# Performance work log

Hardware: AMD Instinct MI355X
Metric: run time of the kernel (lower is better)

## Reference

```python
import jax, jax.numpy as jnp
import numpy as np

B, D_IN, D_STATE, N_SEG = 8192, 2048, 2048, 4


def setup_inputs() -> dict:
    key = jax.random.key(0)
    ks = jax.random.split(key, 7)
    s_in = 1.0 / np.sqrt(D_IN)
    return {
        "x": jax.random.normal(ks[0], (B, D_IN), dtype=jnp.float32),
        "W_seg": jax.random.uniform(ks[1], (N_SEG, D_STATE, D_IN), minval=-s_in, maxval=s_in, dtype=jnp.float32),
        "b_seg": jax.random.uniform(ks[2], (N_SEG, D_STATE), minval=-s_in, maxval=s_in, dtype=jnp.float32),
        "threshold": jnp.zeros((N_SEG, D_STATE), dtype=jnp.float32),
        "W_gate": jax.random.uniform(ks[3], (N_SEG, D_IN), minval=-s_in, maxval=s_in, dtype=jnp.float32),
        "b_gate": jax.random.uniform(ks[4], (N_SEG,), minval=-s_in, maxval=s_in, dtype=jnp.float32),
    }


def reference(x, W_seg, b_seg, threshold, W_gate, b_gate):
    # gates: (B, n_seg)
    gates = jax.nn.sigmoid(x @ W_gate.T + b_gate)
    # all segment projections in one batched GEMM: (n_seg, B, d_state)
    seg = jnp.einsum("bi,sdi->sbd", x, W_seg) + b_seg[:, None, :]
    plateau = jax.nn.sigmoid(5.0 * (seg - threshold[:, None, :]))
    # stacked: (n_seg, B, d_state), gated per segment
    stacked = seg * plateau * gates.T[:, :, None]
    n = stacked.shape[0]
    integrated = (
        stacked.sum(0)
        + 0.1 * jnp.sign(jnp.prod(stacked, 0)) * jnp.power(jnp.prod(jnp.abs(stacked), 0), 1.0 / n)
    )
    return integrated
```

## Files before the change

kernel.cpp:

```cpp
#include <hip/hip_runtime.h>
#include <stdint.h>

#define B_DIM 8192
#define K_DIM 2048
#define N_DIM 2048
#define NSEG 4
#define NT (K_DIM / 64)

typedef int v4i __attribute__((ext_vector_type(4)));

typedef const __attribute__((address_space(1))) void* gas_ptr;
typedef __attribute__((address_space(3))) void* lds_ptr;

__global__ __launch_bounds__(256)
void xquant_gates_kernel(const float* __restrict__ x, const float* __restrict__ Wg,
                         const float* __restrict__ bg, signed char* __restrict__ xq,
                         float* __restrict__ sx, float* __restrict__ gates) {
  const int b = blockIdx.x;
  const int tid = threadIdx.x;
  const size_t base = (size_t)b * K_DIM + tid * 8;
  const float4 v0 = *(const float4*)(x + base);
  const float4 v1 = *(const float4*)(x + base + 4);

  float a[4];
#pragma unroll
  for (int s = 0; s < 4; ++s) {
    const float4 w0 = *(const float4*)(Wg + (size_t)s * K_DIM + tid * 8);
    const float4 w1 = *(const float4*)(Wg + (size_t)s * K_DIM + tid * 8 + 4);
    a[s] = v0.x * w0.x + v0.y * w0.y + v0.z * w0.z + v0.w * w0.w
         + v1.x * w1.x + v1.y * w1.y + v1.z * w1.z + v1.w * w1.w;
  }
  float m = fmaxf(fmaxf(fmaxf(fabsf(v0.x), fabsf(v0.y)), fmaxf(fabsf(v0.z), fabsf(v0.w))),
                  fmaxf(fmaxf(fabsf(v1.x), fabsf(v1.y)), fmaxf(fabsf(v1.z), fabsf(v1.w))));
#pragma unroll
  for (int off = 1; off < 64; off <<= 1) {
    m = fmaxf(m, __shfl_xor(m, off));
#pragma unroll
    for (int s = 0; s < 4; ++s) a[s] += __shfl_xor(a[s], off);
  }
  __shared__ float redg[4][4];
  __shared__ float rmx[4];
  const int wv = tid >> 6;
  if ((tid & 63) == 0) {
    rmx[wv] = m;
#pragma unroll
    for (int s = 0; s < 4; ++s) redg[wv][s] = a[s];
  }
  __syncthreads();
  const float rm = fmaxf(fmaxf(rmx[0], rmx[1]), fmaxf(rmx[2], rmx[3]));
  const float inv = 127.0f / fmaxf(rm, 1e-30f);
  const int q0 = __float2int_rn(v0.x * inv), q1 = __float2int_rn(v0.y * inv);
  const int q2 = __float2int_rn(v0.z * inv), q3 = __float2int_rn(v0.w * inv);
  const int q4 = __float2int_rn(v1.x * inv), q5 = __float2int_rn(v1.y * inv);
  const int q6 = __float2int_rn(v1.z * inv), q7 = __float2int_rn(v1.w * inv);
  const int lo = (q0 & 255) | ((q1 & 255) << 8) | ((q2 & 255) << 16) | ((q3 & 255) << 24);
  const int hi = (q4 & 255) | ((q5 & 255) << 8) | ((q6 & 255) << 16) | ((q7 & 255) << 24);
  ((int2*)xq)[(size_t)b * 256 + tid] = make_int2(lo, hi);
  if (tid == 0) sx[b] = rm * (1.0f / 127.0f);
  if (tid < 4) {
    float v = redg[0][tid] + redg[1][tid] + redg[2][tid] + redg[3][tid] + bg[tid];
    gates[(size_t)b * 4 + tid] = 1.f / (1.f + __expf(-v));
  }
}

__global__ __launch_bounds__(256)
void wquant_kernel(const float* __restrict__ W, signed char* __restrict__ wq,
                   float* __restrict__ sw) {
  const int row = blockIdx.x;
  const int tid = threadIdx.x;
  const size_t base = (size_t)row * K_DIM + tid * 8;
  const float4 v0 = *(const float4*)(W + base);
  const float4 v1 = *(const float4*)(W + base + 4);
  float m = fmaxf(fmaxf(fmaxf(fabsf(v0.x), fabsf(v0.y)), fmaxf(fabsf(v0.z), fabsf(v0.w))),
                  fmaxf(fmaxf(fabsf(v1.x), fabsf(v1.y)), fmaxf(fabsf(v1.z), fabsf(v1.w))));
#pragma unroll
  for (int off = 1; off < 64; off <<= 1) m = fmaxf(m, __shfl_xor(m, off));
  __shared__ float rmx[4];
  if ((tid & 63) == 0) rmx[tid >> 6] = m;
  __syncthreads();
  const float rm = fmaxf(fmaxf(rmx[0], rmx[1]), fmaxf(rmx[2], rmx[3]));
  const float inv = 127.0f / fmaxf(rm, 1e-30f);
  const int q0 = __float2int_rn(v0.x * inv), q1 = __float2int_rn(v0.y * inv);
  const int q2 = __float2int_rn(v0.z * inv), q3 = __float2int_rn(v0.w * inv);
  const int q4 = __float2int_rn(v1.x * inv), q5 = __float2int_rn(v1.y * inv);
  const int q6 = __float2int_rn(v1.z * inv), q7 = __float2int_rn(v1.w * inv);
  const int lo = (q0 & 255) | ((q1 & 255) << 8) | ((q2 & 255) << 16) | ((q3 & 255) << 24);
  const int hi = (q4 & 255) | ((q5 & 255) << 8) | ((q6 & 255) << 16) | ((q7 & 255) << 24);
  ((int2*)wq)[(size_t)row * 256 + tid] = make_int2(lo, hi);
  if (tid == 0) sw[row] = rm * (1.0f / 127.0f);
}

__global__ __launch_bounds__(512, 4)
void seg_gemm_kernel(const signed char* __restrict__ Xq,
                     const signed char* __restrict__ Wq,
                     const float* __restrict__ sx,
                     const float* __restrict__ sw,
                     const float* __restrict__ b_seg,
                     const float* __restrict__ thr,
                     const float* __restrict__ gates,
                     float* __restrict__ out) {
  __shared__ __align__(128) char smem[65536];

  const int tid = threadIdx.x;
  const int lane = tid & 63;
  const int wid = tid >> 6;
  const int wm = wid >> 2;
  const int wn = wid & 3;

  const int id = blockIdx.x;
  const int x = id & 7;
  const int c = id >> 3;
  const int mIdx = (c >> 3) & 7;
  const int nIdx = (c & 7) | ((c >> 6) << 3);
  const int m0 = (x * 8 + mIdx) * 128;
  const int n0 = nIdx * 64;

  const int row_st = tid >> 2;
  const int kc    = (tid & 3) ^ ((tid >> 3) & 3);
  const int keOff = kc * 16;
  const int ldsd  = tid * 16;

  const int l15 = lane & 15;
  const int kg  = lane >> 4;
  const int aSw = l15 * 64 + ((kg ^ ((l15 >> 1) & 3)) << 4);

  v4i acc[NSEG][4];
#pragma unroll
  for (int s = 0; s < NSEG; ++s)
#pragma unroll
    for (int f = 0; f < 4; ++f) acc[s][f] = (v4i){0, 0, 0, 0};

#define STAGE_A(t_) do {                                                            \
    const signed char* s0_ = Xq + (size_t)(m0 + row_st) * K_DIM + (t_) * 64 + keOff; \
    __builtin_amdgcn_global_load_lds((gas_ptr)s0_, (lds_ptr)(smem + ((t_) & 1) * 8192 + ldsd), 16, 0, 0); \
  } while (0)

#define STAGE_B(t_, h_, bb_) do {                                                   \
    const signed char* s0_ = Wq + ((size_t)((h_) * 2 + (tid >> 8)) * N_DIM + (n0 + ((tid >> 2) & 63))) * K_DIM + (t_) * 64 + keOff; \
    __builtin_amdgcn_global_load_lds((gas_ptr)s0_, (lds_ptr)(smem + 16384 + (bb_) * 16384 + (h_) * 8192 + ldsd), 16, 0, 0); \
  } while (0)

#define MFMAI(a_, b_, c_) __builtin_amdgcn_mfma_i32_16x16x64_i8(a_, b_, c_, 0, 0, 0)
#define LD16(p_) (*(const v4i*)(p_))
#define WAITL(n_) asm volatile("s_waitcnt lgkmcnt(" #n_ ")" ::: "memory")

#define MM4(f_) do {                                                                \
    __builtin_amdgcn_s_setprio(1);                                                  \
    acc[0][(f_)] = MFMAI(a[(f_)], bfr[0], acc[0][(f_)]);                            \
    acc[1][(f_)] = MFMAI(a[(f_)], bfr[1], acc[1][(f_)]);                            \
    acc[2][(f_)] = MFMAI(a[(f_)], bfr[2], acc[2][(f_)]);                            \
    acc[3][(f_)] = MFMAI(a[(f_)], bfr[3], acc[3][(f_)]);                            \
    __builtin_amdgcn_s_setprio(0);                                                  \
  } while (0)

  STAGE_A(0);
  STAGE_B(0, 0, 0); STAGE_B(0, 1, 0);
  STAGE_B(1, 0, 1); STAGE_B(1, 1, 1);
  asm volatile("s_waitcnt vmcnt(2)" ::: "memory");
  __builtin_amdgcn_s_barrier();

  int bc = 0, bs = 2;
  for (int t = 0; t < NT; ++t) {
    const char* Ab = smem + (t & 1) * 8192 + wm * 4096;
    const char* Bb = smem + 16384 + bc * 16384;
    v4i bfr[NSEG];
    v4i a[4];

    bfr[0] = LD16(Bb + 0 * 4096 + wn * 1024 + aSw);
    bfr[1] = LD16(Bb + 1 * 4096 + wn * 1024 + aSw);
    bfr[2] = LD16(Bb + 2 * 4096 + wn * 1024 + aSw);
    bfr[3] = LD16(Bb + 3 * 4096 + wn * 1024 + aSw);
    a[0] = LD16(Ab + 0 * 1024 + aSw);
    a[1] = LD16(Ab + 1 * 1024 + aSw);
    a[2] = LD16(Ab + 2 * 1024 + aSw);
    a[3] = LD16(Ab + 3 * 1024 + aSw);
    if (t + 1 < NT) STAGE_A(t + 1);

    WAITL(3);  MM4(0);
    WAITL(2);
    if (t + 2 < NT) STAGE_B(t + 2, 0, bs);
    MM4(1);
    WAITL(1);
    if (t + 2 < NT) STAGE_B(t + 2, 1, bs);
    MM4(2);
    WAITL(0);  MM4(3);

    if (t < NT - 2)      { asm volatile("s_waitcnt vmcnt(2)" ::: "memory"); }
    else if (t == NT - 2){ asm volatile("s_waitcnt vmcnt(0)" ::: "memory"); }
    __builtin_amdgcn_s_barrier();

    bc = (bc == 2) ? 0 : bc + 1;
    bs = (bs == 2) ? 0 : bs + 1;
  }
  asm volatile("s_waitcnt lgkmcnt(0) vmcnt(0)" ::: "memory");

  const int d = n0 + wn * 16 + l15;
  float bsv[NSEG], thv[NSEG], swv[NSEG];
#pragma unroll
  for (int s = 0; s < NSEG; ++s) {
    bsv[s] = b_seg[s * N_DIM + d];
    thv[s] = thr[s * N_DIM + d];
    swv[s] = sw[s * N_DIM + d];
  }
#pragma unroll
  for (int f = 0; f < 4; ++f) {
#pragma unroll
    for (int r = 0; r < 4; ++r) {
      const int brow = m0 + wm * 64 + f * 16 + kg * 4 + r;
      const float sxr = sx[brow];
      const float4 g = *(const float4*)(gates + (size_t)brow * 4);
      const float gv[NSEG] = {g.x, g.y, g.z, g.w};
      float sum = 0.f, prod = 1.f;
#pragma unroll
      for (int s = 0; s < NSEG; ++s) {
        const float seg = (float)acc[s][f][r] * (sxr * swv[s]) + bsv[s];
        const float pl = 1.f / (1.f + __expf(-5.f * (seg - thv[s])));
        const float st = seg * pl * gv[s];
        sum += st;
        prod *= st;
      }
      const float gm = sqrtf(sqrtf(fabsf(prod)));
      out[(size_t)brow * N_DIM + d] = sum + 0.1f * (prod < 0.f ? -gm : gm);
    }
  }
#undef STAGE_A
#undef STAGE_B
#undef MFMAI
#undef LD16
#undef WAITL
#undef MM4
}

extern "C" void kernel_launch(void* const* d_in, const int* in_sizes, int n_in,
                              void* d_out, int out_size, void* d_ws, size_t ws_size,
                              hipStream_t stream) {
  const float* x      = (const float*)d_in[0];
  const float* W_seg  = (const float*)d_in[1];
  const float* b_seg  = (const float*)d_in[2];
  const float* thr    = (const float*)d_in[3];
  const float* W_gate = (const float*)d_in[4];
  const float* b_gate = (const float*)d_in[5];
  float* out = (float*)d_out;

  signed char* xq = (signed char*)d_ws;
  signed char* wq = xq + (size_t)B_DIM * K_DIM;
  float* sx = (float*)(wq + (size_t)NSEG * N_DIM * K_DIM);
  float* sw = sx + B_DIM;
  float* gates = sw + NSEG * N_DIM;

  xquant_gates_kernel<<<B_DIM, 256, 0, stream>>>(x, W_gate, b_gate, xq, sx, gates);
  wquant_kernel<<<NSEG * N_DIM, 256, 0, stream>>>(W_seg, wq, sw);

  seg_gemm_kernel<<<2048, 512, 0, stream>>>(xq, wq, sx, sw, b_seg, thr, gates, out);
}
```

Measured before the change: 219.2 us.

## Load B fragments directly from global into registers, shrink LDS to A only

The weight (B) operand is no longer staged through LDS with global_load_lds. Each lane now reads its 16-byte MFMA fragment straight from global memory into registers, double-buffered across tiles with an unrolled two-tile loop. LDS drops to 16KB holding only the A tiles, which removes the B LDS reads and frees LDS for occupancy. In exchange, B loads are less coalesced (16B per lane strided by K), global-memory latency is exposed in registers, and the MFMA priority hints are removed.

```diff
diff --git a/kernel.cpp b/kernel.cpp
--- a/kernel.cpp
+++ b/kernel.cpp
@@ -99,7 +99,7 @@
                      const float* __restrict__ thr,
                      const float* __restrict__ gates,
                      float* __restrict__ out) {
-  __shared__ __align__(128) char smem[65536];
+  __shared__ __align__(128) char smem[16384];
 
   const int tid = threadIdx.x;
   const int lane = tid & 63;
@@ -115,7 +115,6 @@
   const int m0 = (x * 8 + mIdx) * 128;
   const int n0 = nIdx * 64;
 
-  const int row_st = tid >> 2;
   const int kc    = (tid & 3) ^ ((tid >> 3) & 3);
   const int keOff = kc * 16;
   const int ldsd  = tid * 16;
@@ -124,6 +123,9 @@
   const int kg  = lane >> 4;
   const int aSw = l15 * 64 + ((kg ^ ((l15 >> 1) & 3)) << 4);
 
+  const signed char* wB = Wq + (size_t)(n0 + wn * 16 + l15) * K_DIM + kg * 16;
+#define SEGSTR ((size_t)N_DIM * K_DIM)
+
   v4i acc[NSEG][4];
 #pragma unroll
   for (int s = 0; s < NSEG; ++s)
@@ -131,67 +133,82 @@
     for (int f = 0; f < 4; ++f) acc[s][f] = (v4i){0, 0, 0, 0};
 
 #define STAGE_A(t_) do {                                                            \
-    const signed char* s0_ = Xq + (size_t)(m0 + row_st) * K_DIM + (t_) * 64 + keOff; \
+    const signed char* s0_ = Xq + (size_t)(m0 + (tid >> 2)) * K_DIM + (t_) * 64 + keOff; \
     __builtin_amdgcn_global_load_lds((gas_ptr)s0_, (lds_ptr)(smem + ((t_) & 1) * 8192 + ldsd), 16, 0, 0); \
-  } while (0)
-
-#define STAGE_B(t_, h_, bb_) do {                                                   \
-    const signed char* s0_ = Wq + ((size_t)((h_) * 2 + (tid >> 8)) * N_DIM + (n0 + ((tid >> 2) & 63))) * K_DIM + (t_) * 64 + keOff; \
-    __builtin_amdgcn_global_load_lds((gas_ptr)s0_, (lds_ptr)(smem + 16384 + (bb_) * 16384 + (h_) * 8192 + ldsd), 16, 0, 0); \
   } while (0)
 
 #define MFMAI(a_, b_, c_) __builtin_amdgcn_mfma_i32_16x16x64_i8(a_, b_, c_, 0, 0, 0)
 #define LD16(p_) (*(const v4i*)(p_))
 #define WAITL(n_) asm volatile("s_waitcnt lgkmcnt(" #n_ ")" ::: "memory")
-
-#define MM4(f_) do {                                                                \
-    __builtin_amdgcn_s_setprio(1);                                                  \
-    acc[0][(f_)] = MFMAI(a[(f_)], bfr[0], acc[0][(f_)]);                            \
-    acc[1][(f_)] = MFMAI(a[(f_)], bfr[1], acc[1][(f_)]);                            \
-    acc[2][(f_)] = MFMAI(a[(f_)], bfr[2], acc[2][(f_)]);                            \
-    acc[3][(f_)] = MFMAI(a[(f_)], bfr[3], acc[3][(f_)]);                            \
-    __builtin_amdgcn_s_setprio(0);                                                  \
+#define FENCE asm volatile("" ::: "memory")
+
+#define LOADB(buf_, t_) do {                                                        \
+    buf_[0] = LD16(wB + 0 * SEGSTR + (t_) * 64);                                    \
+    buf_[1] = LD16(wB + 1 * SEGSTR + (t_) * 64);                                    \
+    buf_[2] = LD16(wB + 2 * SEGSTR + (t_) * 64);                                    \
+    buf_[3] = LD16(wB + 3 * SEGSTR + (t_) * 64);                                    \
+  } while (0)
+
+#define MM4(f_, bp_) do {                                                           \
+    acc[0][(f_)] = MFMAI(a[(f_)], bp_[0], acc[0][(f_)]);                            \
+    acc[1][(f_)] = MFMAI(a[(f_)], bp_[1], acc[1][(f_)]);                            \
+    acc[2][(f_)] = MFMAI(a[(f_)], bp_[2], acc[2][(f_)]);                            \
+    acc[3][(f_)] = MFMAI(a[(f_)], bp_[3], acc[3][(f_)]);                            \
+  } while (0)
+
+#define TILE(t_, bcur_, bnext_, LAST_)  do {                                        \
+    const char* Ab_ = smem + ((t_) & 1) * 8192 + wm * 4096;                         \
+    if (!(LAST_)) STAGE_A((t_) + 1);                                                \
+    FENCE;                                                                          \
+    if (!(LAST_) && (t_) + 1 < NT) LOADB(bnext_, (t_) + 1);                         \
+    FENCE;                                                                          \
+    v4i a[4];                                                                       \
+    a[0] = LD16(Ab_ + 0 * 1024 + aSw);                                              \
+    a[1] = LD16(Ab_ + 1 * 1024 + aSw);                                              \
+    a[2] = LD16(Ab_ + 2 * 1024 + aSw);                                              \
+    a[3] = LD16(Ab_ + 3 * 1024 + aSw);                                              \
+    WAITL(3);  MM4(0, bcur_);                                                       \
+    WAITL(2);  MM4(1, bcur_);                                                       \
+    WAITL(1);  MM4(2, bcur_);                                                       \
+    WAITL(0);  MM4(3, bcur_);                                                       \
+    if (!(LAST_)) {                                                                 \
+      asm volatile("s_waitcnt vmcnt(4)" ::: "memory");         \
+      __builtin_amdgcn_s_barrier();                                                 \
+    }                                                                               \
   } while (0)
 
   STAGE_A(0);
-  STAGE_B(0, 0, 0); STAGE_B(0, 1, 0);
-  STAGE_B(1, 0, 1); STAGE_B(1, 1, 1);
-  asm volatile("s_waitcnt vmcnt(2)" ::: "memory");
+  FENCE;
+  v4i bfrA[4], bfrB[4];
+  LOADB(bfrA, 0);
+  FENCE;
+  asm volatile("s_waitcnt vmcnt(4)" ::: "memory");
   __builtin_amdgcn_s_barrier();
 
-  int bc = 0, bs = 2;
-  for (int t = 0; t < NT; ++t) {
-    const char* Ab = smem + (t & 1) * 8192 + wm * 4096;
-    const char* Bb = smem + 16384 + bc * 16384;
-    v4i bfr[NSEG];
+  for (int t = 0; t < NT - 2; t += 2) {
+    TILE(t, bfrA, bfrB, false);
+    TILE(t + 1, bfrB, bfrA, false);
+  }
+  {
+    const int t = NT - 2;
+    const char* Ab_ = smem + (t & 1) * 8192 + wm * 4096;
+    STAGE_A(t + 1);
+    FENCE;
+    LOADB(bfrB, t + 1);
+    FENCE;
     v4i a[4];
-
-    bfr[0] = LD16(Bb + 0 * 4096 + wn * 1024 + aSw);
-    bfr[1] = LD16(Bb + 1 * 4096 + wn * 1024 + aSw);
-    bfr[2] = LD16(Bb + 2 * 4096 + wn * 1024 + aSw);
-    bfr[3] = LD16(Bb + 3 * 4096 + wn * 1024 + aSw);
-    a[0] = LD16(Ab + 0 * 1024 + aSw);
-    a[1] = LD16(Ab + 1 * 1024 + aSw);
-    a[2] = LD16(Ab + 2 * 1024 + aSw);
-    a[3] = LD16(Ab + 3 * 1024 + aSw);
-    if (t + 1 < NT) STAGE_A(t + 1);
-
-    WAITL(3);  MM4(0);
-    WAITL(2);
-    if (t + 2 < NT) STAGE_B(t + 2, 0, bs);
-    MM4(1);
-    WAITL(1);
-    if (t + 2 < NT) STAGE_B(t + 2, 1, bs);
-    MM4(2);
-    WAITL(0);  MM4(3);
-
-    if (t < NT - 2)      { asm volatile("s_waitcnt vmcnt(2)" ::: "memory"); }
-    else if (t == NT - 2){ asm volatile("s_waitcnt vmcnt(0)" ::: "memory"); }
+    a[0] = LD16(Ab_ + 0 * 1024 + aSw);
+    a[1] = LD16(Ab_ + 1 * 1024 + aSw);
+    a[2] = LD16(Ab_ + 2 * 1024 + aSw);
+    a[3] = LD16(Ab_ + 3 * 1024 + aSw);
+    WAITL(3);  MM4(0, bfrA);
+    WAITL(2);  MM4(1, bfrA);
+    WAITL(1);  MM4(2, bfrA);
+    WAITL(0);  MM4(3, bfrA);
+    asm volatile("s_waitcnt vmcnt(4)" ::: "memory");
     __builtin_amdgcn_s_barrier();
-
-    bc = (bc == 2) ? 0 : bc + 1;
-    bs = (bs == 2) ? 0 : bs + 1;
-  }
+  }
+  TILE(NT - 1, bfrB, bfrA, true);
   asm volatile("s_waitcnt lgkmcnt(0) vmcnt(0)" ::: "memory");
 
   const int d = n0 + wn * 16 + l15;
@@ -224,11 +241,14 @@
     }
   }
 #undef STAGE_A
-#undef STAGE_B
 #undef MFMAI
 #undef LD16
 #undef WAITL
+#undef FENCE
+#undef LOADB
 #undef MM4
+#undef TILE
+#undef SEGSTR
 }
 
 extern "C" void kernel_launch(void* const* d_in, const int* in_sizes, int n_in,
```

Result: slower. 326.1 us (+48.8%).

## Load A operand directly from global into registers, bypassing LDS staging

Applied to the files above, without the earlier changes.

The int8 activation tile is no longer staged through LDS. Each wave now reads its A fragments straight from global memory into registers every K-step, and LDS holds only the triple-buffered weight tiles. This cuts LDS use from 64 KB to 48 KB, which may allow more resident blocks, and it removes the A-side LDS writes and reads. The explicit vmcnt waits and MFMA priority hints are also dropped. In exchange the four wn-waves each fetch the same A rows from L2/global with no prefetch, so global load latency now sits on the critical path. Ordering of the asynchronous B loads now depends on the compiler's implicit vmcnt waits.

```diff
diff --git a/kernel.cpp b/kernel.cpp
--- a/kernel.cpp
+++ b/kernel.cpp
@@ -99,7 +99,7 @@
                      const float* __restrict__ thr,
                      const float* __restrict__ gates,
                      float* __restrict__ out) {
-  __shared__ __align__(128) char smem[65536];
+  __shared__ __align__(128) char smem[49152];
 
   const int tid = threadIdx.x;
   const int lane = tid & 63;
@@ -115,7 +115,6 @@
   const int m0 = (x * 8 + mIdx) * 128;
   const int n0 = nIdx * 64;
 
-  const int row_st = tid >> 2;
   const int kc    = (tid & 3) ^ ((tid >> 3) & 3);
   const int keOff = kc * 16;
   const int ldsd  = tid * 16;
@@ -124,36 +123,32 @@
   const int kg  = lane >> 4;
   const int aSw = l15 * 64 + ((kg ^ ((l15 >> 1) & 3)) << 4);
 
+  const signed char* wA = Xq + (size_t)(m0 + wm * 64 + l15) * K_DIM + kg * 16;
+#define AROW ((size_t)16 * K_DIM)
+
   v4i acc[NSEG][4];
 #pragma unroll
   for (int s = 0; s < NSEG; ++s)
 #pragma unroll
     for (int f = 0; f < 4; ++f) acc[s][f] = (v4i){0, 0, 0, 0};
-
-#define STAGE_A(t_) do {                                                            \
-    const signed char* s0_ = Xq + (size_t)(m0 + row_st) * K_DIM + (t_) * 64 + keOff; \
-    __builtin_amdgcn_global_load_lds((gas_ptr)s0_, (lds_ptr)(smem + ((t_) & 1) * 8192 + ldsd), 16, 0, 0); \
-  } while (0)
 
 #define STAGE_B(t_, h_, bb_) do {                                                   \
     const signed char* s0_ = Wq + ((size_t)((h_) * 2 + (tid >> 8)) * N_DIM + (n0 + ((tid >> 2) & 63))) * K_DIM + (t_) * 64 + keOff; \
-    __builtin_amdgcn_global_load_lds((gas_ptr)s0_, (lds_ptr)(smem + 16384 + (bb_) * 16384 + (h_) * 8192 + ldsd), 16, 0, 0); \
+    __builtin_amdgcn_global_load_lds((gas_ptr)s0_, (lds_ptr)(smem + (bb_) * 16384 + (h_) * 8192 + ldsd), 16, 0, 0); \
   } while (0)
 
 #define MFMAI(a_, b_, c_) __builtin_amdgcn_mfma_i32_16x16x64_i8(a_, b_, c_, 0, 0, 0)
 #define LD16(p_) (*(const v4i*)(p_))
 #define WAITL(n_) asm volatile("s_waitcnt lgkmcnt(" #n_ ")" ::: "memory")
+#define FENCE asm volatile("" ::: "memory")
 
 #define MM4(f_) do {                                                                \
-    __builtin_amdgcn_s_setprio(1);                                                  \
     acc[0][(f_)] = MFMAI(a[(f_)], bfr[0], acc[0][(f_)]);                            \
     acc[1][(f_)] = MFMAI(a[(f_)], bfr[1], acc[1][(f_)]);                            \
     acc[2][(f_)] = MFMAI(a[(f_)], bfr[2], acc[2][(f_)]);                            \
     acc[3][(f_)] = MFMAI(a[(f_)], bfr[3], acc[3][(f_)]);                            \
-    __builtin_amdgcn_s_setprio(0);                                                  \
   } while (0)
 
-  STAGE_A(0);
   STAGE_B(0, 0, 0); STAGE_B(0, 1, 0);
   STAGE_B(1, 0, 1); STAGE_B(1, 1, 1);
   asm volatile("s_waitcnt vmcnt(2)" ::: "memory");
@@ -161,32 +156,29 @@
 
   int bc = 0, bs = 2;
   for (int t = 0; t < NT; ++t) {
-    const char* Ab = smem + (t & 1) * 8192 + wm * 4096;
-    const char* Bb = smem + 16384 + bc * 16384;
+    const char* Bb = smem + bc * 16384;
     v4i bfr[NSEG];
     v4i a[4];
+
+    const signed char* aT = wA + t * 64;
+    a[0] = LD16(aT + 0 * AROW);
+    a[1] = LD16(aT + 1 * AROW);
+    a[2] = LD16(aT + 2 * AROW);
+    a[3] = LD16(aT + 3 * AROW);
+    FENCE;
+    if (t + 2 < NT) { STAGE_B(t + 2, 0, bs); STAGE_B(t + 2, 1, bs); }
+    FENCE;
 
     bfr[0] = LD16(Bb + 0 * 4096 + wn * 1024 + aSw);
     bfr[1] = LD16(Bb + 1 * 4096 + wn * 1024 + aSw);
     bfr[2] = LD16(Bb + 2 * 4096 + wn * 1024 + aSw);
     bfr[3] = LD16(Bb + 3 * 4096 + wn * 1024 + aSw);
-    a[0] = LD16(Ab + 0 * 1024 + aSw);
-    a[1] = LD16(Ab + 1 * 1024 + aSw);
-    a[2] = LD16(Ab + 2 * 1024 + aSw);
-    a[3] = LD16(Ab + 3 * 1024 + aSw);
-    if (t + 1 < NT) STAGE_A(t + 1);
 
     WAITL(3);  MM4(0);
-    WAITL(2);
-    if (t + 2 < NT) STAGE_B(t + 2, 0, bs);
-    MM4(1);
-    WAITL(1);
-    if (t + 2 < NT) STAGE_B(t + 2, 1, bs);
-    MM4(2);
+    WAITL(2);  MM4(1);
+    WAITL(1);  MM4(2);
     WAITL(0);  MM4(3);
 
-    if (t < NT - 2)      { asm volatile("s_waitcnt vmcnt(2)" ::: "memory"); }
-    else if (t == NT - 2){ asm volatile("s_waitcnt vmcnt(0)" ::: "memory"); }
     __builtin_amdgcn_s_barrier();
 
     bc = (bc == 2) ? 0 : bc + 1;
@@ -223,12 +215,13 @@
       out[(size_t)brow * N_DIM + d] = sum + 0.1f * (prod < 0.f ? -gm : gm);
     }
   }
-#undef STAGE_A
 #undef STAGE_B
 #undef MFMAI
 #undef LD16
 #undef WAITL
+#undef FENCE
 #undef MM4
+#undef AROW
 }
 
 extern "C" void kernel_launch(void* const* d_in, const int* in_sizes, int n_in,
```

New measurement: 329.1 us. 1.5x slower.
